# Optimization experiments

Hardware: AMD Instinct MI355X
Metric: run time of the kernel (lower is better)

## Reference

```python
import jax, jax.numpy as jnp
import numpy as np

EPS = 1e-8
LN_EPS = 1e-5
DIM, NHEADS = 512, 8
HEAD_DIM = DIM // NHEADS
SCALE = HEAD_DIM ** -0.5
ROLE_VOCAB = 8


def _layernorm(x, g, b):
    mu = x.mean(-1, keepdims=True)
    var = ((x - mu) ** 2).mean(-1, keepdims=True)
    return (x - mu) * jax.lax.rsqrt(var + LN_EPS) * g + b


def setup_inputs() -> dict:
    key = jax.random.key(0)
    ks = jax.random.split(key, 16)
    B, K, L, D = 8, 4, 1024, DIM
    s = 1.0 / np.sqrt(D)
    return {
        "state_repr": jax.random.normal(ks[0], (B, K, L, D), jnp.float32),
        "residue_mask": jax.random.randint(ks[1], (B, K, L), 0, 2) > 0,
        "state_weights": jax.random.uniform(ks[2], (B, K), jnp.float32),
        "state_roles": jax.random.randint(ks[3], (B, K), 0, ROLE_VOCAB),
        "state_present_mask": jnp.ones((B, K), dtype=bool),
        "role_emb": jax.random.normal(ks[4], (ROLE_VOCAB, D), jnp.float32),
        "Wq": jax.random.normal(ks[5], (D, D), jnp.float32) * s,
        "Wk": jax.random.normal(ks[6], (D, D), jnp.float32) * s,
        "Wv": jax.random.normal(ks[7], (D, D), jnp.float32) * s,
        "Wo": jax.random.normal(ks[8], (D, D), jnp.float32) * s,
        "ln1_g": jnp.ones((3 * D,), jnp.float32),
        "ln1_b": jnp.zeros((3 * D,), jnp.float32),
        "Wg1": jax.random.normal(ks[9], (D, 3 * D), jnp.float32) / np.sqrt(3 * D),
        "bg1": jnp.zeros((D,), jnp.float32),
        "Wg2": jax.random.normal(ks[10], (D, D), jnp.float32) * s,
        "bg2": jnp.zeros((D,), jnp.float32),
        "norm_g": jnp.ones((D,), jnp.float32),
        "norm_b": jnp.zeros((D,), jnp.float32),
    }


def _forward(state_repr, residue_mask, state_weights, state_roles, state_present_mask,
             role_emb, Wq, Wk, Wv, Wo, ln1_g, ln1_b, Wg1, bg1, Wg2, bg2, norm_g, norm_b):
    B, K, L, D = state_repr.shape
    H, hd = NHEADS, HEAD_DIM
    roles = jnp.maximum(state_roles, 0)
    role_e = role_emb[roles][:, :, None, :]                       # [B,K,1,D]
    valid = residue_mask & state_present_mask[:, :, None]          # [B,K,L]

    # normalized state weights
    pres = state_present_mask.astype(jnp.float32)
    w = state_weights.astype(jnp.float32) * pres
    denom = w.sum(1, keepdims=True)
    fallback = pres / jnp.maximum(pres.sum(1, keepdims=True), 1.0)
    nsw = jnp.where(denom > EPS, w / jnp.maximum(denom, EPS), fallback)  # [B,K]

    x = (state_repr + role_e) * valid[..., None]
    x = x.transpose(0, 2, 1, 3)                                    # [B,L,K,D]
    valid_rlk = valid.transpose(0, 2, 1)                           # [B,L,K]

    def proj(W):  # torch Linear: y = x @ W.T
        return (x @ W.T).reshape(B, L, K, H, hd).transpose(0, 1, 3, 2, 4)  # [B,L,H,K,hd]

    q, k, v = proj(Wq), proj(Wk), proj(Wv)
    logits = jnp.einsum('blhqd,blhkd->blhqk', q, k) * SCALE
    logits = logits + jnp.log(jnp.maximum(nsw, EPS))[:, None, None, None, :]
    key_mask = valid_rlk[:, :, None, None, :]                      # [B,L,1,1,K]
    logits = jnp.where(key_mask, logits, -jnp.inf)
    attn = jax.nn.softmax(logits, axis=-1)
    attn = jnp.nan_to_num(attn, nan=0.0, posinf=0.0, neginf=0.0)
    attn_out = jnp.einsum('blhqk,blhkd->blhqd', attn, v)
    attn_out = attn_out.transpose(0, 1, 3, 2, 4).reshape(B, L, K, D)
    attn_out = (attn_out @ Wo.T) * valid_rlk[..., None]

    swr = nsw[:, None, :] * valid_rlk.astype(jnp.float32)          # [B,L,K]
    swr = swr / jnp.maximum(swr.sum(-1, keepdims=True), EPS)
    weighted_mean = jnp.sum(x * swr[..., None], axis=2)            # [B,L,D]
    attn_pooled = jnp.sum(attn_out * swr[..., None], axis=2)

    max_in = jnp.where(valid_rlk[..., None], x, -1e9)
    max_feat = max_in.max(axis=2)
    has_any = valid_rlk.any(axis=2, keepdims=True)
    max_feat = jnp.where(has_any, max_feat, 0.0)

    fusion_base = 0.5 * (attn_pooled + weighted_mean)
    gate_in = jnp.concatenate([attn_pooled, weighted_mean, max_feat], axis=-1)
    h = _layernorm(gate_in, ln1_g, ln1_b)
    h = jax.nn.gelu(h @ Wg1.T + bg1, approximate=False)
    gate = jax.nn.sigmoid(h @ Wg2.T + bg2)
    fused = gate * fusion_base + (1.0 - gate) * max_feat
    fused = _layernorm(fused + weighted_mean, norm_g, norm_b)

    attn_mean = attn.mean(axis=(2, 3))                             # [B,L,K]
    return fused, attn_pooled, weighted_mean, max_feat, attn_mean, nsw


def reference(state_repr, residue_mask, state_weights, state_roles, state_present_mask,
              role_emb, Wq, Wk, Wv, Wo, ln1_g, ln1_b, Wg1, bg1, Wg2, bg2, norm_g, norm_b):
    return _forward(state_repr, residue_mask, state_weights, state_roles, state_present_mask,
                    role_emb, Wq, Wk, Wv, Wo, ln1_g, ln1_b, Wg1, bg1, Wg2, bg2, norm_g, norm_b)
```

## Files before the change

### kernel.cpp

```cpp
#include <hip/hip_runtime.h>
#include <math.h>

#define BB 8
#define KK 4
#define LL 1024
#define DD 512
#define HD 64
#define D3 1536
#define MM (BB*LL*KK)
#define BL (BB*LL)
#define SCALE 0.125f
#define EPSF 1e-8f
#define LN_EPSF 1e-5f

typedef _Float16 hfrag __attribute__((ext_vector_type(8)));
typedef float f32x4 __attribute__((ext_vector_type(4)));

__device__ __forceinline__ unsigned short f2h(float f) {
    _Float16 h = (_Float16)f;
    unsigned short u; __builtin_memcpy(&u, &h, 2); return u;
}
__device__ __forceinline__ float h2f(unsigned short u) {
    _Float16 h; __builtin_memcpy(&h, &u, 2); return (float)h;
}

__device__ __forceinline__ void glds16(const unsigned short* g, unsigned short* l) {
    __builtin_amdgcn_global_load_lds(
        (const __attribute__((address_space(1))) void*)g,
        (__attribute__((address_space(3))) void*)l, 16, 0, 0);
}

__device__ __forceinline__ void nsw_compute(const float* sw, const int* pres,
                                            int b, float* nswv) {
    float w[KK], pr[KK]; float denom = 0.f, ps = 0.f;
    #pragma unroll
    for (int k = 0; k < KK; ++k) {
        pr[k] = pres[b*KK + k] ? 1.f : 0.f;
        w[k]  = sw[b*KK + k] * pr[k];
        denom += w[k]; ps += pr[k];
    }
    #pragma unroll
    for (int k = 0; k < KK; ++k)
        nswv[k] = (denom > EPSF) ? w[k] / fmaxf(denom, EPSF)
                                 : pr[k] / fmaxf(ps, 1.f);
}

#define WSZ 262144
#define OG1 1048576
#define OG2 1835008
#define WTOT 2097152
__global__ __launch_bounds__(256) void cvt_weights(
        const float* __restrict__ Wq, const float* __restrict__ Wk,
        const float* __restrict__ Wv, const float* __restrict__ Wo,
        const float* __restrict__ Wg1, const float* __restrict__ Wg2,
        unsigned short* __restrict__ dst) {
    int t = blockIdx.x * 256 + threadIdx.x;
    int e = t * 4;
    const float* src; int off;
    if      (e < WSZ)    { src = Wq;  off = e; }
    else if (e < 2*WSZ)  { src = Wk;  off = e - WSZ; }
    else if (e < 3*WSZ)  { src = Wv;  off = e - 2*WSZ; }
    else if (e < OG1)    { src = Wo;  off = e - 3*WSZ; }
    else if (e < OG2)    { src = Wg1; off = e - OG1; }
    else                 { src = Wg2; off = e - OG2; }
    float4 v = *(const float4*)(src + off);
    ushort4 o;
    o.x = f2h(v.x); o.y = f2h(v.y); o.z = f2h(v.z); o.w = f2h(v.w);
    *(ushort4*)(dst + e) = o;
}

__global__ __launch_bounds__(256) void buildx_kernel(
        const float* __restrict__ SR, const int* __restrict__ residue,
        const int* __restrict__ pres, const int* __restrict__ roles,
        const float* __restrict__ role_emb, const float* __restrict__ sw,
        unsigned short* __restrict__ Xh, float* __restrict__ rowmask,
        float* __restrict__ out_wm, float* __restrict__ out_mx,
        float* __restrict__ f_nsw) {
    int t  = blockIdx.x * 256 + threadIdx.x;
    int bl = t >> 7;
    int d4 = (t & 127) << 2;
    int b  = bl >> 10, l = bl & 1023;
    float nswv[KK];
    nsw_compute(sw, pres, b, nswv);
    float mk[KK], swr[KK];
    float ssum = 0.f, many = 0.f;
    #pragma unroll
    for (int k = 0; k < KK; ++k) {
        int bk = b*KK + k;
        bool valid = (residue[(size_t)bk*LL + l] != 0) && (pres[bk] != 0);
        mk[k]  = valid ? 1.f : 0.f;
        swr[k] = nswv[k] * mk[k];
        ssum += swr[k]; many += mk[k];
    }
    float inv = 1.f / fmaxf(ssum, EPSF);
    bool hasany = many > 0.5f;
    float wmx = 0.f, wmy = 0.f, wmz = 0.f, wmw = 0.f;
    float mxx = -1e9f, mxy = -1e9f, mxz = -1e9f, mxw = -1e9f;
    #pragma unroll
    for (int k = 0; k < KK; ++k) {
        int bk = b*KK + k;
        int role = roles[bk]; if (role < 0) role = 0;
        float4 sr = *(const float4*)(SR + ((size_t)bk*LL + l)*DD + d4);
        float4 re = *(const float4*)(role_emb + (size_t)role*DD + d4);
        float xx = (sr.x + re.x)*mk[k], xy = (sr.y + re.y)*mk[k];
        float xz = (sr.z + re.z)*mk[k], xw = (sr.w + re.w)*mk[k];
        ushort4 xs; xs.x = f2h(xx); xs.y = f2h(xy); xs.z = f2h(xz); xs.w = f2h(xw);
        *(ushort4*)(Xh + (size_t)(bl*KK + k)*DD + d4) = xs;
        float s = swr[k]*inv;
        wmx = fmaf(xx, s, wmx); wmy = fmaf(xy, s, wmy);
        wmz = fmaf(xz, s, wmz); wmw = fmaf(xw, s, wmw);
        if (mk[k] > 0.5f) {
            mxx = fmaxf(mxx, xx); mxy = fmaxf(mxy, xy);
            mxz = fmaxf(mxz, xz); mxw = fmaxf(mxw, xw);
        }
    }
    if (!hasany) { mxx = mxy = mxz = mxw = 0.f; }
    float4 wmv; wmv.x = wmx; wmv.y = wmy; wmv.z = wmz; wmv.w = wmw;
    float4 mxv; mxv.x = mxx; mxv.y = mxy; mxv.z = mxz; mxv.w = mxw;
    *(float4*)(out_wm + (size_t)bl*DD + d4) = wmv;
    *(float4*)(out_mx + (size_t)bl*DD + d4) = mxv;
    if (d4 == 0) {
        #pragma unroll
        for (int k = 0; k < KK; ++k) rowmask[bl*KK + k] = mk[k];
    }
    if (blockIdx.x == 0 && threadIdx.x < BB*KK) {
        int bb = threadIdx.x >> 2, kk2 = threadIdx.x & 3;
        float nv[KK];
        nsw_compute(sw, pres, bb, nv);
        f_nsw[threadIdx.x] = nv[kk2];
    }
}

__global__ __launch_bounds__(512, 4) void gemm_qkv_8p(
        const unsigned short* __restrict__ A, const unsigned short* __restrict__ W,
        unsigned short* __restrict__ Cbase) {
    __shared__ __align__(16) unsigned short smem[36864];
    const int tid  = threadIdx.x;
    const int wave = tid >> 6, lane = tid & 63;
    const int id = blockIdx.x;
    const int wg = (id & 7) * 192 + (id >> 3);
    const int m0 = (wg / 12) * 256;
    const int n0 = (wg % 12) * 128;
    const int wm = wave >> 1, wn = wave & 1;
    const int fr = lane & 15, q = lane >> 4;
    const int srow = tid >> 2, scc = tid & 3;
    const int sswz = (scc ^ ((srow >> 1) & 3)) << 3;
    const unsigned short* Ag0 = A + (size_t)(m0 + srow)*512 + sswz;
    const unsigned short* Ag1 = Ag0 + (size_t)128*512;
    const unsigned short* Wg0 = W + (size_t)(n0 + srow)*512 + sswz;
    const int lA0 = tid << 3;
    const int lA1 = (tid + 512) << 3;
    int aoff[4], boff[4];
    #pragma unroll
    for (int mf = 0; mf < 4; ++mf) {
        int row = (wm << 6) + (mf << 4) + fr;
        aoff[mf] = (row << 5) + ((q ^ ((row >> 1) & 3)) << 3);
    }
    #pragma unroll
    for (int nf = 0; nf < 4; ++nf) {
        int row = (wn << 6) + (nf << 4) + fr;
        boff[nf] = (row << 5) + ((q ^ ((row >> 1) & 3)) << 3);
    }
    f32x4 acc[4][4] = {};

#define VMWAIT(N) asm volatile("s_waitcnt vmcnt(" #N ")" ::: "memory")
#define STAGE(tt) do { unsigned short* _d = smem + ((tt) % 3) * 12288; \
        const int _ko = (tt) << 5; \
        glds16(Ag0 + _ko, _d + lA0); glds16(Ag1 + _ko, _d + lA1); \
        glds16(Wg0 + _ko, _d + 8192 + lA0); } while (0)
#define MFROW(ai, areg) \
        acc[ai][0] = __builtin_amdgcn_mfma_f32_16x16x32_f16(areg, b0, acc[ai][0], 0, 0, 0); \
        acc[ai][1] = __builtin_amdgcn_mfma_f32_16x16x32_f16(areg, b1, acc[ai][1], 0, 0, 0); \
        acc[ai][2] = __builtin_amdgcn_mfma_f32_16x16x32_f16(areg, b2, acc[ai][2], 0, 0, 0); \
        acc[ai][3] = __builtin_amdgcn_mfma_f32_16x16x32_f16(areg, b3, acc[ai][3], 0, 0, 0);
#define TILE(t, STG, VM) do { \
        const unsigned short* _Ab = smem + ((t) % 3) * 12288; \
        const unsigned short* _Bb = _Ab + 8192; \
        VMWAIT(VM); \
        __builtin_amdgcn_s_barrier(); \
        __builtin_amdgcn_sched_barrier(0); \
        hfrag b0 = *(const hfrag*)(_Bb + boff[0]); \
        hfrag b1 = *(const hfrag*)(_Bb + boff[1]); \
        hfrag b2 = *(const hfrag*)(_Bb + boff[2]); \
        hfrag b3 = *(const hfrag*)(_Bb + boff[3]); \
        hfrag a0_ = *(const hfrag*)(_Ab + aoff[0]); \
        hfrag a1_ = *(const hfrag*)(_Ab + aoff[1]); \
        hfrag a2_ = *(const hfrag*)(_Ab + aoff[2]); \
        hfrag a3_ = *(const hfrag*)(_Ab + aoff[3]); \
        if (STG) STAGE((t) + 2); \
        __builtin_amdgcn_s_setprio(1); \
        MFROW(0, a0_) MFROW(1, a1_) MFROW(2, a2_) MFROW(3, a3_) \
        __builtin_amdgcn_s_setprio(0); \
    } while (0)

    STAGE(0); STAGE(1);
    #pragma unroll
    for (int t = 0; t < 14; ++t) TILE(t, 1, 3);
    TILE(14, 0, 3);
    TILE(15, 0, 0);
#undef TILE
#undef MFROW
#undef STAGE
#undef VMWAIT

    const int gc0 = n0 + (wn << 6);
    const int seg = gc0 >> 9;
    unsigned short* Cs = Cbase + (size_t)seg * ((size_t)MM * 512);
    const int cb = gc0 & 511;
    #pragma unroll
    for (int mf = 0; mf < 4; ++mf) {
        const int grow = m0 + (wm << 6) + (mf << 4) + (q << 2);
        #pragma unroll
        for (int nf = 0; nf < 4; ++nf) {
            const int col = cb + (nf << 4) + fr;
            #pragma unroll
            for (int r = 0; r < 4; ++r)
                Cs[(size_t)(grow + r) * 512 + col] = f2h(acc[mf][nf][r]);
        }
    }
}

__global__ __launch_bounds__(256) void attn_kernel(
        const unsigned short* __restrict__ Qb, const unsigned short* __restrict__ Kb,
        const unsigned short* __restrict__ Vb,
        unsigned short* __restrict__ pooled,
        const float* __restrict__ sw, const int* __restrict__ pres,
        const float* __restrict__ rowmask,
        float* __restrict__ attn_mean_out) {
    __shared__ float att[128];
    __shared__ float wv[32];
    __shared__ float lw[KK], mk[KK], sp[KK];
    int bl = blockIdx.x, b = bl >> 10, mb = bl * KK;
    int tid = threadIdx.x;
    if (tid < KK) {
        float nv[KK];
        nsw_compute(sw, pres, b, nv);
        lw[tid] = logf(fmaxf(nv[tid], EPSF));
        float mkk[KK]; float ssum = 0.f;
        #pragma unroll
        for (int k = 0; k < KK; ++k) { mkk[k] = rowmask[mb + k]; ssum += nv[k]*mkk[k]; }
        mk[tid] = mkk[tid];
        sp[tid] = nv[tid]*mkk[tid] / fmaxf(ssum, EPSF);
    }
    __syncthreads();
    if (tid < 128) {
        int h = tid >> 4, i = (tid >> 2) & 3, j = tid & 3;
        const unsigned short* qp = Qb + (size_t)(mb + i)*DD + h*HD;
        const unsigned short* kp = Kb + (size_t)(mb + j)*DD + h*HD;
        float s = 0.f;
        #pragma unroll
        for (int c = 0; c < 8; ++c) {
            hfrag qv = *(const hfrag*)(qp + c*8);
            hfrag kv = *(const hfrag*)(kp + c*8);
            #pragma unroll
            for (int e = 0; e < 8; ++e)
                s = fmaf((float)qv[e], (float)kv[e], s);
        }
        float lg = s * SCALE + lw[j];
        att[tid] = (mk[j] > 0.5f) ? lg : -INFINITY;
    }
    __syncthreads();
    if (tid < 32) {
        int base = tid * 4;
        float l0 = att[base], l1 = att[base+1], l2 = att[base+2], l3 = att[base+3];
        float m = fmaxf(fmaxf(l0, l1), fmaxf(l2, l3));
        if (m == -INFINITY) {
            att[base] = att[base+1] = att[base+2] = att[base+3] = 0.f;
        } else {
            float e0 = expf(l0 - m), e1 = expf(l1 - m), e2 = expf(l2 - m), e3 = expf(l3 - m);
            float inv = 1.f / (e0 + e1 + e2 + e3);
            att[base] = e0*inv; att[base+1] = e1*inv; att[base+2] = e2*inv; att[base+3] = e3*inv;
        }
    }
    __syncthreads();
    if (tid < KK) {
        float s = 0.f;
        for (int hi = 0; hi < 32; ++hi) s += att[hi*4 + tid];
        attn_mean_out[(size_t)bl*KK + tid] = s * (1.f/32.f);
    }
    if (tid < 32) {
        int h = tid >> 2, j = tid & 3;
        wv[tid] = sp[0]*att[h*16 + 0*4 + j] + sp[1]*att[h*16 + 1*4 + j]
                + sp[2]*att[h*16 + 2*4 + j] + sp[3]*att[h*16 + 3*4 + j];
    }
    __syncthreads();
    {
        int d2 = tid << 1, h = d2 >> 6;
        float s0 = 0.f, s1 = 0.f;
        #pragma unroll
        for (int j = 0; j < KK; ++j) {
            float aj = wv[h*4 + j];
            ushort2 vvv = *(const ushort2*)(Vb + (size_t)(mb + j)*DD + d2);
            s0 = fmaf(aj, h2f(vvv.x), s0);
            s1 = fmaf(aj, h2f(vvv.y), s1);
        }
        ushort2 o; o.x = f2h(s0); o.y = f2h(s1);
        *(ushort2*)(pooled + (size_t)bl*DD + d2) = o;
    }
}

__global__ __launch_bounds__(256, 3) void ap_gemm(
        const unsigned short* __restrict__ A,
        const unsigned short* __restrict__ W,
        float* __restrict__ out_ap) {
    __shared__ __align__(16) unsigned short smem[24576];
    const int tid  = threadIdx.x;
    const int wave = tid >> 6, lane = tid & 63;
    const int id = blockIdx.x;
    const int wg = (id & 7) * 32 + (id >> 3);
    const int m0 = (wg >> 2) * 128;
    const int n0 = (wg & 3) * 128;
    const int wm = wave >> 1, wn = wave & 1;
    const int fr = lane & 15, q = lane >> 4;
    const int srow = tid >> 2, scc = tid & 3;
    const int sswz = (scc ^ ((srow >> 1) & 3)) << 3;
    const unsigned short* Ag0 = A + (size_t)(m0 + srow)*512 + sswz;
    const unsigned short* Ag1 = Ag0 + (size_t)64*512;
    const unsigned short* Wg0 = W + (size_t)(n0 + srow)*512 + sswz;
    const unsigned short* Wg1p = Wg0 + (size_t)64*512;
    const int lA0 = tid << 3;
    const int lA1 = (tid + 256) << 3;
    int aoff[4], boff[4];
    #pragma unroll
    for (int mf = 0; mf < 4; ++mf) {
        int row = (wm << 6) + (mf << 4) + fr;
        aoff[mf] = (row << 5) + ((q ^ ((row >> 1) & 3)) << 3);
    }
    #pragma unroll
    for (int nf = 0; nf < 4; ++nf) {
        int row = (wn << 6) + (nf << 4) + fr;
        boff[nf] = (row << 5) + ((q ^ ((row >> 1) & 3)) << 3);
    }
    f32x4 acc[4][4] = {};

#define VMWAIT(N) asm volatile("s_waitcnt vmcnt(" #N ")" ::: "memory")
#define STAGE(tt) do { unsigned short* _d = smem + ((tt) % 3) * 8192; \
        const int _ko = (tt) << 5; \
        glds16(Ag0 + _ko, _d + lA0); glds16(Ag1 + _ko, _d + lA1); \
        glds16(Wg0 + _ko, _d + 4096 + lA0); glds16(Wg1p + _ko, _d + 4096 + lA1); } while (0)
#define MFROW(ai, areg) \
        acc[ai][0] = __builtin_amdgcn_mfma_f32_16x16x32_f16(areg, b0, acc[ai][0], 0, 0, 0); \
        acc[ai][1] = __builtin_amdgcn_mfma_f32_16x16x32_f16(areg, b1, acc[ai][1], 0, 0, 0); \
        acc[ai][2] = __builtin_amdgcn_mfma_f32_16x16x32_f16(areg, b2, acc[ai][2], 0, 0, 0); \
        acc[ai][3] = __builtin_amdgcn_mfma_f32_16x16x32_f16(areg, b3, acc[ai][3], 0, 0, 0);
#define TILE(t, STG, VM) do { \
        const unsigned short* _Ab = smem + ((t) % 3) * 8192; \
        const unsigned short* _Bb = _Ab + 4096; \
        VMWAIT(VM); \
        __builtin_amdgcn_s_barrier(); \
        __builtin_amdgcn_sched_barrier(0); \
        hfrag b0 = *(const hfrag*)(_Bb + boff[0]); \
        hfrag b1 = *(const hfrag*)(_Bb + boff[1]); \
        hfrag b2 = *(const hfrag*)(_Bb + boff[2]); \
        hfrag b3 = *(const hfrag*)(_Bb + boff[3]); \
        hfrag a0_ = *(const hfrag*)(_Ab + aoff[0]); \
        hfrag a1_ = *(const hfrag*)(_Ab + aoff[1]); \
        hfrag a2_ = *(const hfrag*)(_Ab + aoff[2]); \
        hfrag a3_ = *(const hfrag*)(_Ab + aoff[3]); \
        if (STG) STAGE((t) + 2); \
        __builtin_amdgcn_s_setprio(1); \
        MFROW(0, a0_) MFROW(1, a1_) MFROW(2, a2_) MFROW(3, a3_) \
        __builtin_amdgcn_s_setprio(0); \
    } while (0)

    STAGE(0); STAGE(1);
    #pragma unroll
    for (int t = 0; t < 14; ++t) TILE(t, 1, 4);
    TILE(14, 0, 4);
    TILE(15, 0, 0);
#undef TILE
#undef MFROW
#undef STAGE
#undef VMWAIT

    #pragma unroll
    for (int mf = 0; mf < 4; ++mf) {
        const int grow = m0 + (wm << 6) + (mf << 4) + (q << 2);
        #pragma unroll
        for (int nf = 0; nf < 4; ++nf) {
            const int col = n0 + (wn << 6) + (nf << 4) + fr;
            #pragma unroll
            for (int r = 0; r < 4; ++r)
                out_ap[(size_t)(grow + r)*512 + col] = acc[mf][nf][r];
        }
    }
}

__global__ __launch_bounds__(256) void ln1_kernel(
        const float* __restrict__ ap, const float* __restrict__ wm,
        const float* __restrict__ mx, const float* __restrict__ g,
        const float* __restrict__ bvec, unsigned short* __restrict__ hin) {
    const int bl = blockIdx.x * 4 + (threadIdx.x >> 6);
    const int lane = threadIdx.x & 63;
    const int c0 = lane * 8;
    float4 v[3][2];
    const float* srcs[3] = { ap + (size_t)bl*512 + c0,
                             wm + (size_t)bl*512 + c0,
                             mx + (size_t)bl*512 + c0 };
    float s = 0.f, s2 = 0.f;
    #pragma unroll
    for (int sg = 0; sg < 3; ++sg) {
        v[sg][0] = *(const float4*)(srcs[sg]);
        v[sg][1] = *(const float4*)(srcs[sg] + 4);
        #pragma unroll
        for (int e = 0; e < 8; ++e) {
            float x = ((const float*)v[sg])[e];
            s += x; s2 += x*x;
        }
    }
    #pragma unroll
    for (int o = 1; o < 64; o <<= 1) {
        s  += __shfl_xor(s,  o, 64);
        s2 += __shfl_xor(s2, o, 64);
    }
    const float mu = s * (1.f/(float)D3);
    const float var = s2 * (1.f/(float)D3) - mu*mu;
    const float rstd = rsqrtf(var + LN_EPSF);
    #pragma unroll
    for (int sg = 0; sg < 3; ++sg) {
        const int gofs = sg*512 + c0;
        #pragma unroll
        for (int h = 0; h < 2; ++h) {
            float4 g4 = *(const float4*)(g + gofs + h*4);
            float4 b4 = *(const float4*)(bvec + gofs + h*4);
            const float* sv = (const float*)&v[sg][h];
            ushort4 o4;
            o4.x = f2h((sv[0]-mu)*rstd*g4.x + b4.x);
            o4.y = f2h((sv[1]-mu)*rstd*g4.y + b4.y);
            o4.z = f2h((sv[2]-mu)*rstd*g4.z + b4.z);
            o4.w = f2h((sv[3]-mu)*rstd*g4.w + b4.w);
            *(ushort4*)(hin + (size_t)bl*D3 + gofs + h*4) = o4;
        }
    }
}

__global__ __launch_bounds__(256, 3) void gemm_g1(
        const unsigned short* __restrict__ A, const unsigned short* __restrict__ W,
        unsigned short* __restrict__ C, const float* __restrict__ bias) {
    __shared__ __align__(16) unsigned short smem[24576];
    const int tid  = threadIdx.x;
    const int wave = tid >> 6, lane = tid & 63;
    const int id = blockIdx.x;
    const int wg = (id & 7) * 32 + (id >> 3);
    const int m0 = (wg >> 2) * 128;
    const int n0 = (wg & 3) * 128;
    const int wm = wave >> 1, wn = wave & 1;
    const int fr = lane & 15, q = lane >> 4;
    const int srow = tid >> 2, scc = tid & 3;
    const int sswz = (scc ^ ((srow >> 1) & 3)) << 3;
    const unsigned short* Ag0 = A + (size_t)(m0 + srow)*D3 + sswz;
    const unsigned short* Ag1 = Ag0 + (size_t)64*D3;
    const unsigned short* Wg0 = W + (size_t)(n0 + srow)*D3 + sswz;
    const unsigned short* Wg1p = Wg0 + (size_t)64*D3;
    const int lA0 = tid << 3;
    const int lA1 = (tid + 256) << 3;
    int aoff[4], boff[4];
    #pragma unroll
    for (int mf = 0; mf < 4; ++mf) {
        int row = (wm << 6) + (mf << 4) + fr;
        aoff[mf] = (row << 5) + ((q ^ ((row >> 1) & 3)) << 3);
    }
    #pragma unroll
    for (int nf = 0; nf < 4; ++nf) {
        int row = (wn << 6) + (nf << 4) + fr;
        boff[nf] = (row << 5) + ((q ^ ((row >> 1) & 3)) << 3);
    }
    f32x4 acc[4][4] = {};

#define VMWAIT(N) asm volatile("s_waitcnt vmcnt(" #N ")" ::: "memory")
#define STAGE(tt) do { unsigned short* _d = smem + ((tt) % 3) * 8192; \
        const int _ko = (tt) << 5; \
        glds16(Ag0 + _ko, _d + lA0); glds16(Ag1 + _ko, _d + lA1); \
        glds16(Wg0 + _ko, _d + 4096 + lA0); glds16(Wg1p + _ko, _d + 4096 + lA1); } while (0)
#define MFROW(ai, areg) \
        acc[ai][0] = __builtin_amdgcn_mfma_f32_16x16x32_f16(areg, b0, acc[ai][0], 0, 0, 0); \
        acc[ai][1] = __builtin_amdgcn_mfma_f32_16x16x32_f16(areg, b1, acc[ai][1], 0, 0, 0); \
        acc[ai][2] = __builtin_amdgcn_mfma_f32_16x16x32_f16(areg, b2, acc[ai][2], 0, 0, 0); \
        acc[ai][3] = __builtin_amdgcn_mfma_f32_16x16x32_f16(areg, b3, acc[ai][3], 0, 0, 0);
#define TILE(t, STG, VM) do { \
        const unsigned short* _Ab = smem + ((t) % 3) * 8192; \
        const unsigned short* _Bb = _Ab + 4096; \
        VMWAIT(VM); \
        __builtin_amdgcn_s_barrier(); \
        __builtin_amdgcn_sched_barrier(0); \
        hfrag b0 = *(const hfrag*)(_Bb + boff[0]); \
        hfrag b1 = *(const hfrag*)(_Bb + boff[1]); \
        hfrag b2 = *(const hfrag*)(_Bb + boff[2]); \
        hfrag b3 = *(const hfrag*)(_Bb + boff[3]); \
        hfrag a0_ = *(const hfrag*)(_Ab + aoff[0]); \
        hfrag a1_ = *(const hfrag*)(_Ab + aoff[1]); \
        hfrag a2_ = *(const hfrag*)(_Ab + aoff[2]); \
        hfrag a3_ = *(const hfrag*)(_Ab + aoff[3]); \
        if (STG) STAGE((t) + 2); \
        __builtin_amdgcn_s_setprio(1); \
        MFROW(0, a0_) MFROW(1, a1_) MFROW(2, a2_) MFROW(3, a3_) \
        __builtin_amdgcn_s_setprio(0); \
    } while (0)

    STAGE(0); STAGE(1);
    #pragma unroll 3
    for (int t = 0; t < 46; ++t) TILE(t, 1, 4);
    TILE(46, 0, 4);
    TILE(47, 0, 0);
#undef TILE
#undef MFROW
#undef STAGE
#undef VMWAIT

    #pragma unroll
    for (int mf = 0; mf < 4; ++mf) {
        const int grow = m0 + (wm << 6) + (mf << 4) + (q << 2);
        #pragma unroll
        for (int nf = 0; nf < 4; ++nf) {
            const int col = n0 + (wn << 6) + (nf << 4) + fr;
            const float bv = bias[col];
            #pragma unroll
            for (int r = 0; r < 4; ++r) {
                float v = acc[mf][nf][r] + bv;
                v = 0.5f * v * (1.f + erff(v * 0.70710678118654752f));
                C[(size_t)(grow + r) * 512 + col] = f2h(v);
            }
        }
    }
}

__global__ __launch_bounds__(256, 3) void wg2_gemm(
        const unsigned short* __restrict__ A,
        const unsigned short* __restrict__ W,
        const float* __restrict__ bg2,
        const float* __restrict__ in_ap, const float* __restrict__ in_wm,
        const float* __restrict__ in_mx, float* __restrict__ pre) {
    __shared__ __align__(16) unsigned short smem[24576];
    const int tid  = threadIdx.x;
    const int wave = tid >> 6, lane = tid & 63;
    const int id = blockIdx.x;
    const int wg = (id & 7) * 32 + (id >> 3);
    const int m0 = (wg >> 2) * 128;
    const int n0 = (wg & 3) * 128;
    const int wm = wave >> 1, wn = wave & 1;
    const int fr = lane & 15, q = lane >> 4;
    const int srow = tid >> 2, scc = tid & 3;
    const int sswz = (scc ^ ((srow >> 1) & 3)) << 3;
    const unsigned short* Ag0 = A + (size_t)(m0 + srow)*512 + sswz;
    const unsigned short* Ag1 = Ag0 + (size_t)64*512;
    const unsigned short* Wg0 = W + (size_t)(n0 + srow)*512 + sswz;
    const unsigned short* Wg1p = Wg0 + (size_t)64*512;
    const int lA0 = tid << 3;
    const int lA1 = (tid + 256) << 3;
    int aoff[4], boff[4];
    #pragma unroll
    for (int mf = 0; mf < 4; ++mf) {
        int row = (wm << 6) + (mf << 4) + fr;
        aoff[mf] = (row << 5) + ((q ^ ((row >> 1) & 3)) << 3);
    }
    #pragma unroll
    for (int nf = 0; nf < 4; ++nf) {
        int row = (wn << 6) + (nf << 4) + fr;
        boff[nf] = (row << 5) + ((q ^ ((row >> 1) & 3)) << 3);
    }
    f32x4 acc[4][4] = {};

#define VMWAIT(N) asm volatile("s_waitcnt vmcnt(" #N ")" ::: "memory")
#define STAGE(tt) do { unsigned short* _d = smem + ((tt) % 3) * 8192; \
        const int _ko = (tt) << 5; \
        glds16(Ag0 + _ko, _d + lA0); glds16(Ag1 + _ko, _d + lA1); \
        glds16(Wg0 + _ko, _d + 4096 + lA0); glds16(Wg1p + _ko, _d + 4096 + lA1); } while (0)
#define MFROW(ai, areg) \
        acc[ai][0] = __builtin_amdgcn_mfma_f32_16x16x32_f16(areg, b0, acc[ai][0], 0, 0, 0); \
        acc[ai][1] = __builtin_amdgcn_mfma_f32_16x16x32_f16(areg, b1, acc[ai][1], 0, 0, 0); \
        acc[ai][2] = __builtin_amdgcn_mfma_f32_16x16x32_f16(areg, b2, acc[ai][2], 0, 0, 0); \
        acc[ai][3] = __builtin_amdgcn_mfma_f32_16x16x32_f16(areg, b3, acc[ai][3], 0, 0, 0);
#define TILE(t, STG, VM) do { \
        const unsigned short* _Ab = smem + ((t) % 3) * 8192; \
        const unsigned short* _Bb = _Ab + 4096; \
        VMWAIT(VM); \
        __builtin_amdgcn_s_barrier(); \
        __builtin_amdgcn_sched_barrier(0); \
        hfrag b0 = *(const hfrag*)(_Bb + boff[0]); \
        hfrag b1 = *(const hfrag*)(_Bb + boff[1]); \
        hfrag b2 = *(const hfrag*)(_Bb + boff[2]); \
        hfrag b3 = *(const hfrag*)(_Bb + boff[3]); \
        hfrag a0_ = *(const hfrag*)(_Ab + aoff[0]); \
        hfrag a1_ = *(const hfrag*)(_Ab + aoff[1]); \
        hfrag a2_ = *(const hfrag*)(_Ab + aoff[2]); \
        hfrag a3_ = *(const hfrag*)(_Ab + aoff[3]); \
        if (STG) STAGE((t) + 2); \
        __builtin_amdgcn_s_setprio(1); \
        MFROW(0, a0_) MFROW(1, a1_) MFROW(2, a2_) MFROW(3, a3_) \
        __builtin_amdgcn_s_setprio(0); \
    } while (0)

    STAGE(0); STAGE(1);
    #pragma unroll
    for (int t = 0; t < 14; ++t) TILE(t, 1, 4);
    TILE(14, 0, 4);
    TILE(15, 0, 0);
#undef TILE
#undef MFROW
#undef STAGE
#undef VMWAIT

    #pragma unroll
    for (int mf = 0; mf < 4; ++mf) {
        const int grow = m0 + (wm << 6) + (mf << 4) + (q << 2);
        #pragma unroll
        for (int nf = 0; nf < 4; ++nf) {
            const int col = n0 + (wn << 6) + (nf << 4) + fr;
            const float bv = bg2[col];
            #pragma unroll
            for (int r = 0; r < 4; ++r) {
                const int row = grow + r;
                float g = 1.f / (1.f + expf(-(acc[mf][nf][r] + bv)));
                float ap = in_ap[(size_t)row*512 + col];
                float wmv = in_wm[(size_t)row*512 + col];
                float mxv = in_mx[(size_t)row*512 + col];
                pre[(size_t)row*512 + col] = g*0.5f*(ap + wmv) + (1.f - g)*mxv + wmv;
            }
        }
    }
}

__global__ __launch_bounds__(256) void final_ln_kernel(
        const float* __restrict__ pre, const float* __restrict__ ng,
        const float* __restrict__ nb, float* __restrict__ fused) {
    const int row = blockIdx.x * 4 + (threadIdx.x >> 6);
    const int lane = threadIdx.x & 63;
    const int c0 = lane * 8;
    float4 p0 = *(const float4*)(pre + (size_t)row*512 + c0);
    float4 p1 = *(const float4*)(pre + (size_t)row*512 + c0 + 4);
    float s = 0.f, s2 = 0.f;
    const float* pv = (const float*)&p0;
    #pragma unroll
    for (int e = 0; e < 4; ++e) { s += pv[e]; s2 += pv[e]*pv[e]; }
    pv = (const float*)&p1;
    #pragma unroll
    for (int e = 0; e < 4; ++e) { s += pv[e]; s2 += pv[e]*pv[e]; }
    #pragma unroll
    for (int o = 1; o < 64; o <<= 1) {
        s  += __shfl_xor(s,  o, 64);
        s2 += __shfl_xor(s2, o, 64);
    }
    const float mu = s * (1.f/(float)DD);
    const float var = s2 * (1.f/(float)DD) - mu*mu;
    const float rstd = rsqrtf(var + LN_EPSF);
    float4 g0 = *(const float4*)(ng + c0), g1 = *(const float4*)(ng + c0 + 4);
    float4 b0 = *(const float4*)(nb + c0), b1 = *(const float4*)(nb + c0 + 4);
    float4 o0, o1;
    o0.x = (p0.x-mu)*rstd*g0.x + b0.x; o0.y = (p0.y-mu)*rstd*g0.y + b0.y;
    o0.z = (p0.z-mu)*rstd*g0.z + b0.z; o0.w = (p0.w-mu)*rstd*g0.w + b0.w;
    o1.x = (p1.x-mu)*rstd*g1.x + b1.x; o1.y = (p1.y-mu)*rstd*g1.y + b1.y;
    o1.z = (p1.z-mu)*rstd*g1.z + b1.z; o1.w = (p1.w-mu)*rstd*g1.w + b1.w;
    *(float4*)(fused + (size_t)row*512 + c0) = o0;
    *(float4*)(fused + (size_t)row*512 + c0 + 4) = o1;
}

extern "C" void kernel_launch(void* const* d_in, const int* in_sizes, int n_in,
                              void* d_out, int out_size, void* d_ws, size_t ws_size,
                              hipStream_t stream) {
    const float* SR      = (const float*)d_in[0];
    const int*   residue = (const int*)d_in[1];
    const float* sw      = (const float*)d_in[2];
    const int*   roles   = (const int*)d_in[3];
    const int*   pres    = (const int*)d_in[4];
    const float* role_emb= (const float*)d_in[5];
    const float* Wq      = (const float*)d_in[6];
    const float* Wk      = (const float*)d_in[7];
    const float* Wv      = (const float*)d_in[8];
    const float* Wo      = (const float*)d_in[9];
    const float* ln1_g   = (const float*)d_in[10];
    const float* ln1_b   = (const float*)d_in[11];
    const float* Wg1     = (const float*)d_in[12];
    const float* bg1     = (const float*)d_in[13];
    const float* Wg2     = (const float*)d_in[14];
    const float* bg2     = (const float*)d_in[15];
    const float* norm_g  = (const float*)d_in[16];
    const float* norm_b  = (const float*)d_in[17];

    float* out = (float*)d_out;
    const size_t BLD = (size_t)BL * DD;
    float* f_fused = out;
    float* f_ap    = out + BLD;
    float* f_wm    = out + 2*BLD;
    float* f_mx    = out + 3*BLD;
    float* f_am    = out + 4*BLD;
    float* f_nsw   = out + 4*BLD + (size_t)BL*KK;

    char* base = (char*)d_ws;
    const size_t MD2 = (size_t)MM * DD * 2;
    unsigned short* Xh = (unsigned short*)(base);
    unsigned short* Qh = (unsigned short*)(base + MD2);
    unsigned short* Kh = (unsigned short*)(base + 2*MD2);
    unsigned short* Vh = (unsigned short*)(base + 3*MD2);
    unsigned short* Wb = (unsigned short*)(base + 4*MD2);
    float* rmask = (float*)(base + 4*MD2 + (size_t)WTOT*2);
    unsigned short* PVh  = Xh;
    unsigned short* Hin  = Vh;
    unsigned short* Hbuf = Xh;
    float* preb = (float*)Kh;
    const unsigned short* Wqkv = Wb;
    const unsigned short* Woh  = Wb + 3*WSZ;
    const unsigned short* Wg1h = Wb + OG1;
    const unsigned short* Wg2h = Wb + OG2;

    dim3 blk(256);

    cvt_weights<<<WTOT/1024, blk, 0, stream>>>(Wq, Wk, Wv, Wo, Wg1, Wg2, Wb);
    buildx_kernel<<<(BL*128)/256, blk, 0, stream>>>(SR, residue, pres, roles, role_emb,
                                                    sw, Xh, rmask, f_wm, f_mx, f_nsw);

    gemm_qkv_8p<<<dim3(1536), dim3(512), 0, stream>>>(Xh, Wqkv, Qh);

    attn_kernel<<<BL, blk, 0, stream>>>(Qh, Kh, Vh, PVh, sw, pres, rmask, f_am);

    ap_gemm<<<dim3(256), blk, 0, stream>>>(PVh, Woh, f_ap);

    ln1_kernel<<<dim3(BL/4), blk, 0, stream>>>(
        f_ap, f_wm, f_mx, ln1_g, ln1_b, Hin);

    gemm_g1<<<dim3(256), blk, 0, stream>>>(Hin, Wg1h, Hbuf, bg1);

    wg2_gemm<<<dim3(256), blk, 0, stream>>>(
        Hbuf, Wg2h, bg2, f_ap, f_wm, f_mx, preb);

    final_ln_kernel<<<dim3(BL/4), blk, 0, stream>>>(
        preb, norm_g, norm_b, f_fused);
}
```

Baseline: 314.3 us.

## Use 64x64 tiles for the three tail GEMMs and batch two rows per attention block

Replaces the three 128x128-tile tail GEMMs (output projection, gate layer 1, gate layer 2) with one templated 64x64-tile kernel that launches 1024 blocks instead of 256. The aim is to fill all compute units of the MI355X, since 256 blocks leave many CUs idle. The attention kernel now handles two (b,l) rows per block so all 256 threads do work, and the V pooling uses wider loads. Smaller tiles give less data reuse per block and put more pressure on global and L2 bandwidth.

```diff
diff --git a/kernel.cpp b/kernel.cpp
--- a/kernel.cpp
+++ b/kernel.cpp
@@ -220,6 +220,101 @@
     }
 }
 
+template<int KT, int EPI>
+__global__ __launch_bounds__(256, 4) void gemm_tail(
+        const unsigned short* __restrict__ A, const unsigned short* __restrict__ W,
+        void* __restrict__ Cv, const float* __restrict__ bias,
+        const float* __restrict__ in_ap, const float* __restrict__ in_wm,
+        const float* __restrict__ in_mx) {
+    constexpr int K = KT * 32;
+    __shared__ __align__(16) unsigned short smem[12288];
+    const int tid  = threadIdx.x;
+    const int wave = tid >> 6, lane = tid & 63;
+    const int id = blockIdx.x;
+    const int wg = (id & 7) * 128 + (id >> 3);
+    const int m0 = (wg >> 3) * 64;
+    const int n0 = (wg & 7) * 64;
+    const int wm = wave >> 1, wn = wave & 1;
+    const int fr = lane & 15, q = lane >> 4;
+    const int srow = tid >> 2, scc = tid & 3;
+    const int sswz = (scc ^ ((srow >> 1) & 3)) << 3;
+    const unsigned short* Ag = A + (size_t)(m0 + srow)*K + sswz;
+    const unsigned short* Wg = W + (size_t)(n0 + srow)*K + sswz;
+    const int lA = tid << 3;
+    const int lB = 2048 + (tid << 3);
+    int aoff[2], boff[2];
+    #pragma unroll
+    for (int mf = 0; mf < 2; ++mf) {
+        int row = (wm << 5) + (mf << 4) + fr;
+        aoff[mf] = (row << 5) + ((q ^ ((row >> 1) & 3)) << 3);
+    }
+    #pragma unroll
+    for (int nf = 0; nf < 2; ++nf) {
+        int row = (wn << 5) + (nf << 4) + fr;
+        boff[nf] = 2048 + (row << 5) + ((q ^ ((row >> 1) & 3)) << 3);
+    }
+    f32x4 acc[2][2] = {};
+
+#define VMWAIT(N) asm volatile("s_waitcnt vmcnt(" #N ")" ::: "memory")
+#define STAGE(tt) do { unsigned short* _d = smem + ((tt) % 3) * 4096; \
+        const int _ko = (tt) << 5; \
+        glds16(Ag + _ko, _d + lA); glds16(Wg + _ko, _d + lB); } while (0)
+#define TILE(t, STG, VM) do { \
+        const unsigned short* _Ab = smem + ((t) % 3) * 4096; \
+        VMWAIT(VM); \
+        __builtin_amdgcn_s_barrier(); \
+        __builtin_amdgcn_sched_barrier(0); \
+        hfrag b0 = *(const hfrag*)(_Ab + boff[0]); \
+        hfrag b1 = *(const hfrag*)(_Ab + boff[1]); \
+        hfrag a0_ = *(const hfrag*)(_Ab + aoff[0]); \
+        hfrag a1_ = *(const hfrag*)(_Ab + aoff[1]); \
+        if (STG) STAGE((t) + 2); \
+        __builtin_amdgcn_s_setprio(1); \
+        acc[0][0] = __builtin_amdgcn_mfma_f32_16x16x32_f16(a0_, b0, acc[0][0], 0, 0, 0); \
+        acc[0][1] = __builtin_amdgcn_mfma_f32_16x16x32_f16(a0_, b1, acc[0][1], 0, 0, 0); \
+        acc[1][0] = __builtin_amdgcn_mfma_f32_16x16x32_f16(a1_, b0, acc[1][0], 0, 0, 0); \
+        acc[1][1] = __builtin_amdgcn_mfma_f32_16x16x32_f16(a1_, b1, acc[1][1], 0, 0, 0); \
+        __builtin_amdgcn_s_setprio(0); \
+    } while (0)
+
+    STAGE(0); STAGE(1);
+    #pragma unroll 3
+    for (int t = 0; t < KT - 2; ++t) TILE(t, 1, 2);
+    TILE(KT - 2, 0, 2);
+    TILE(KT - 1, 0, 0);
+#undef TILE
+#undef STAGE
+#undef VMWAIT
+
+    #pragma unroll
+    for (int mf = 0; mf < 2; ++mf) {
+        const int grow = m0 + (wm << 5) + (mf << 4) + (q << 2);
+        #pragma unroll
+        for (int nf = 0; nf < 2; ++nf) {
+            const int col = n0 + (wn << 5) + (nf << 4) + fr;
+            #pragma unroll
+            for (int r = 0; r < 4; ++r) {
+                const int row = grow + r;
+                float v = acc[mf][nf][r];
+                if (EPI == 0) {
+                    ((float*)Cv)[(size_t)row*512 + col] = v;
+                } else if (EPI == 1) {
+                    v += bias[col];
+                    v = 0.5f * v * (1.f + erff(v * 0.70710678118654752f));
+                    ((unsigned short*)Cv)[(size_t)row*512 + col] = f2h(v);
+                } else {
+                    float g = 1.f / (1.f + expf(-(v + bias[col])));
+                    float ap = in_ap[(size_t)row*512 + col];
+                    float wmv = in_wm[(size_t)row*512 + col];
+                    float mxv = in_mx[(size_t)row*512 + col];
+                    ((float*)Cv)[(size_t)row*512 + col] =
+                        g*0.5f*(ap + wmv) + (1.f - g)*mxv + wmv;
+                }
+            }
+        }
+    }
+}
+
 __global__ __launch_bounds__(256) void attn_kernel(
         const unsigned short* __restrict__ Qb, const unsigned short* __restrict__ Kb,
         const unsigned short* __restrict__ Vb,
@@ -227,24 +322,31 @@
         const float* __restrict__ sw, const int* __restrict__ pres,
         const float* __restrict__ rowmask,
         float* __restrict__ attn_mean_out) {
-    __shared__ float att[128];
-    __shared__ float wv[32];
-    __shared__ float lw[KK], mk[KK], sp[KK];
-    int bl = blockIdx.x, b = bl >> 10, mb = bl * KK;
-    int tid = threadIdx.x;
-    if (tid < KK) {
+    __shared__ float att[2][128];
+    __shared__ float wv[2][32];
+    __shared__ float lw[2][KK], mk[2][KK], sp[2][KK];
+    const int blp = blockIdx.x * 2;
+    const int tid = threadIdx.x;
+    if (tid < 8) {
+        const int blq = tid >> 2, k = tid & 3;
+        const int bl = blp + blq, b = bl >> 10;
         float nv[KK];
         nsw_compute(sw, pres, b, nv);
-        lw[tid] = logf(fmaxf(nv[tid], EPSF));
+        lw[blq][k] = logf(fmaxf(nv[k], EPSF));
         float mkk[KK]; float ssum = 0.f;
         #pragma unroll
-        for (int k = 0; k < KK; ++k) { mkk[k] = rowmask[mb + k]; ssum += nv[k]*mkk[k]; }
-        mk[tid] = mkk[tid];
-        sp[tid] = nv[tid]*mkk[tid] / fmaxf(ssum, EPSF);
+        for (int kk = 0; kk < KK; ++kk) {
+            mkk[kk] = rowmask[bl*KK + kk];
+            ssum += nv[kk]*mkk[kk];
+        }
+        mk[blq][k] = mkk[k];
+        sp[blq][k] = nv[k]*mkk[k] / fmaxf(ssum, EPSF);
     }
     __syncthreads();
-    if (tid < 128) {
-        int h = tid >> 4, i = (tid >> 2) & 3, j = tid & 3;
+    {
+        const int blq = tid >> 7, t2 = tid & 127;
+        const int h = t2 >> 4, i = (t2 >> 2) & 3, j = t2 & 3;
+        const int mb = (blp + blq) * KK;
         const unsigned short* qp = Qb + (size_t)(mb + i)*DD + h*HD;
         const unsigned short* kp = Kb + (size_t)(mb + j)*DD + h*HD;
         float s = 0.f;
@@ -256,133 +358,55 @@
             for (int e = 0; e < 8; ++e)
                 s = fmaf((float)qv[e], (float)kv[e], s);
         }
-        float lg = s * SCALE + lw[j];
-        att[tid] = (mk[j] > 0.5f) ? lg : -INFINITY;
+        float lg = s * SCALE + lw[blq][j];
+        att[blq][t2] = (mk[blq][j] > 0.5f) ? lg : -INFINITY;
     }
     __syncthreads();
-    if (tid < 32) {
-        int base = tid * 4;
-        float l0 = att[base], l1 = att[base+1], l2 = att[base+2], l3 = att[base+3];
+    if (tid < 64) {
+        const int blq = tid >> 5, t2 = tid & 31;
+        float* ab = &att[blq][t2 * 4];
+        float l0 = ab[0], l1 = ab[1], l2 = ab[2], l3 = ab[3];
         float m = fmaxf(fmaxf(l0, l1), fmaxf(l2, l3));
         if (m == -INFINITY) {
-            att[base] = att[base+1] = att[base+2] = att[base+3] = 0.f;
+            ab[0] = ab[1] = ab[2] = ab[3] = 0.f;
         } else {
             float e0 = expf(l0 - m), e1 = expf(l1 - m), e2 = expf(l2 - m), e3 = expf(l3 - m);
             float inv = 1.f / (e0 + e1 + e2 + e3);
-            att[base] = e0*inv; att[base+1] = e1*inv; att[base+2] = e2*inv; att[base+3] = e3*inv;
+            ab[0] = e0*inv; ab[1] = e1*inv; ab[2] = e2*inv; ab[3] = e3*inv;
         }
     }
     __syncthreads();
-    if (tid < KK) {
+    if (tid < 8) {
+        const int blq = tid >> 2, k = tid & 3;
         float s = 0.f;
-        for (int hi = 0; hi < 32; ++hi) s += att[hi*4 + tid];
-        attn_mean_out[(size_t)bl*KK + tid] = s * (1.f/32.f);
-    }
-    if (tid < 32) {
-        int h = tid >> 2, j = tid & 3;
-        wv[tid] = sp[0]*att[h*16 + 0*4 + j] + sp[1]*att[h*16 + 1*4 + j]
-                + sp[2]*att[h*16 + 2*4 + j] + sp[3]*att[h*16 + 3*4 + j];
+        for (int hi = 0; hi < 32; ++hi) s += att[blq][hi*4 + k];
+        attn_mean_out[(size_t)(blp + blq)*KK + k] = s * (1.f/32.f);
+    }
+    if (tid < 64) {
+        const int blq = tid >> 5, t2 = tid & 31;
+        const int h = t2 >> 2, j = t2 & 3;
+        wv[blq][t2] = sp[blq][0]*att[blq][h*16 + 0*4 + j]
+                    + sp[blq][1]*att[blq][h*16 + 1*4 + j]
+                    + sp[blq][2]*att[blq][h*16 + 2*4 + j]
+                    + sp[blq][3]*att[blq][h*16 + 3*4 + j];
     }
     __syncthreads();
     {
-        int d2 = tid << 1, h = d2 >> 6;
-        float s0 = 0.f, s1 = 0.f;
+        const int blq = tid >> 7, t2 = tid & 127;
+        const int d4 = t2 << 2, h = d4 >> 6;
+        const int mb = (blp + blq) * KK;
+        float s0 = 0.f, s1 = 0.f, s2 = 0.f, s3 = 0.f;
         #pragma unroll
         for (int j = 0; j < KK; ++j) {
-            float aj = wv[h*4 + j];
-            ushort2 vvv = *(const ushort2*)(Vb + (size_t)(mb + j)*DD + d2);
-            s0 = fmaf(aj, h2f(vvv.x), s0);
-            s1 = fmaf(aj, h2f(vvv.y), s1);
-        }
-        ushort2 o; o.x = f2h(s0); o.y = f2h(s1);
-        *(ushort2*)(pooled + (size_t)bl*DD + d2) = o;
-    }
-}
-
-__global__ __launch_bounds__(256, 3) void ap_gemm(
-        const unsigned short* __restrict__ A,
-        const unsigned short* __restrict__ W,
-        float* __restrict__ out_ap) {
-    __shared__ __align__(16) unsigned short smem[24576];
-    const int tid  = threadIdx.x;
-    const int wave = tid >> 6, lane = tid & 63;
-    const int id = blockIdx.x;
-    const int wg = (id & 7) * 32 + (id >> 3);
-    const int m0 = (wg >> 2) * 128;
-    const int n0 = (wg & 3) * 128;
-    const int wm = wave >> 1, wn = wave & 1;
-    const int fr = lane & 15, q = lane >> 4;
-    const int srow = tid >> 2, scc = tid & 3;
-    const int sswz = (scc ^ ((srow >> 1) & 3)) << 3;
-    const unsigned short* Ag0 = A + (size_t)(m0 + srow)*512 + sswz;
-    const unsigned short* Ag1 = Ag0 + (size_t)64*512;
-    const unsigned short* Wg0 = W + (size_t)(n0 + srow)*512 + sswz;
-    const unsigned short* Wg1p = Wg0 + (size_t)64*512;
-    const int lA0 = tid << 3;
-    const int lA1 = (tid + 256) << 3;
-    int aoff[4], boff[4];
-    #pragma unroll
-    for (int mf = 0; mf < 4; ++mf) {
-        int row = (wm << 6) + (mf << 4) + fr;
-        aoff[mf] = (row << 5) + ((q ^ ((row >> 1) & 3)) << 3);
-    }
-    #pragma unroll
-    for (int nf = 0; nf < 4; ++nf) {
-        int row = (wn << 6) + (nf << 4) + fr;
-        boff[nf] = (row << 5) + ((q ^ ((row >> 1) & 3)) << 3);
-    }
-    f32x4 acc[4][4] = {};
-
-#define VMWAIT(N) asm volatile("s_waitcnt vmcnt(" #N ")" ::: "memory")
-#define STAGE(tt) do { unsigned short* _d = smem + ((tt) % 3) * 8192; \
-        const int _ko = (tt) << 5; \
-        glds16(Ag0 + _ko, _d + lA0); glds16(Ag1 + _ko, _d + lA1); \
-        glds16(Wg0 + _ko, _d + 4096 + lA0); glds16(Wg1p + _ko, _d + 4096 + lA1); } while (0)
-#define MFROW(ai, areg) \
-        acc[ai][0] = __builtin_amdgcn_mfma_f32_16x16x32_f16(areg, b0, acc[ai][0], 0, 0, 0); \
-        acc[ai][1] = __builtin_amdgcn_mfma_f32_16x16x32_f16(areg, b1, acc[ai][1], 0, 0, 0); \
-        acc[ai][2] = __builtin_amdgcn_mfma_f32_16x16x32_f16(areg, b2, acc[ai][2], 0, 0, 0); \
-        acc[ai][3] = __builtin_amdgcn_mfma_f32_16x16x32_f16(areg, b3, acc[ai][3], 0, 0, 0);
-#define TILE(t, STG, VM) do { \
-        const unsigned short* _Ab = smem + ((t) % 3) * 8192; \
-        const unsigned short* _Bb = _Ab + 4096; \
-        VMWAIT(VM); \
-        __builtin_amdgcn_s_barrier(); \
-        __builtin_amdgcn_sched_barrier(0); \
-        hfrag b0 = *(const hfrag*)(_Bb + boff[0]); \
-        hfrag b1 = *(const hfrag*)(_Bb + boff[1]); \
-        hfrag b2 = *(const hfrag*)(_Bb + boff[2]); \
-        hfrag b3 = *(const hfrag*)(_Bb + boff[3]); \
-        hfrag a0_ = *(const hfrag*)(_Ab + aoff[0]); \
-        hfrag a1_ = *(const hfrag*)(_Ab + aoff[1]); \
-        hfrag a2_ = *(const hfrag*)(_Ab + aoff[2]); \
-        hfrag a3_ = *(const hfrag*)(_Ab + aoff[3]); \
-        if (STG) STAGE((t) + 2); \
-        __builtin_amdgcn_s_setprio(1); \
-        MFROW(0, a0_) MFROW(1, a1_) MFROW(2, a2_) MFROW(3, a3_) \
-        __builtin_amdgcn_s_setprio(0); \
-    } while (0)
-
-    STAGE(0); STAGE(1);
-    #pragma unroll
-    for (int t = 0; t < 14; ++t) TILE(t, 1, 4);
-    TILE(14, 0, 4);
-    TILE(15, 0, 0);
-#undef TILE
-#undef MFROW
-#undef STAGE
-#undef VMWAIT
-
-    #pragma unroll
-    for (int mf = 0; mf < 4; ++mf) {
-        const int grow = m0 + (wm << 6) + (mf << 4) + (q << 2);
-        #pragma unroll
-        for (int nf = 0; nf < 4; ++nf) {
-            const int col = n0 + (wn << 6) + (nf << 4) + fr;
-            #pragma unroll
-            for (int r = 0; r < 4; ++r)
-                out_ap[(size_t)(grow + r)*512 + col] = acc[mf][nf][r];
-        }
+            float aj = wv[blq][h*4 + j];
+            ushort4 vv = *(const ushort4*)(Vb + (size_t)(mb + j)*DD + d4);
+            s0 = fmaf(aj, h2f(vv.x), s0);
+            s1 = fmaf(aj, h2f(vv.y), s1);
+            s2 = fmaf(aj, h2f(vv.z), s2);
+            s3 = fmaf(aj, h2f(vv.w), s3);
+        }
+        ushort4 o; o.x = f2h(s0); o.y = f2h(s1); o.z = f2h(s2); o.w = f2h(s3);
+        *(ushort4*)(pooled + (size_t)(blp + blq)*DD + d4) = o;
     }
 }
 
@@ -430,192 +454,6 @@
             o4.z = f2h((sv[2]-mu)*rstd*g4.z + b4.z);
             o4.w = f2h((sv[3]-mu)*rstd*g4.w + b4.w);
             *(ushort4*)(hin + (size_t)bl*D3 + gofs + h*4) = o4;
-        }
-    }
-}
-
-__global__ __launch_bounds__(256, 3) void gemm_g1(
-        const unsigned short* __restrict__ A, const unsigned short* __restrict__ W,
-        unsigned short* __restrict__ C, const float* __restrict__ bias) {
-    __shared__ __align__(16) unsigned short smem[24576];
-    const int tid  = threadIdx.x;
-    const int wave = tid >> 6, lane = tid & 63;
-    const int id = blockIdx.x;
-    const int wg = (id & 7) * 32 + (id >> 3);
-    const int m0 = (wg >> 2) * 128;
-    const int n0 = (wg & 3) * 128;
-    const int wm = wave >> 1, wn = wave & 1;
-    const int fr = lane & 15, q = lane >> 4;
-    const int srow = tid >> 2, scc = tid & 3;
-    const int sswz = (scc ^ ((srow >> 1) & 3)) << 3;
-    const unsigned short* Ag0 = A + (size_t)(m0 + srow)*D3 + sswz;
-    const unsigned short* Ag1 = Ag0 + (size_t)64*D3;
-    const unsigned short* Wg0 = W + (size_t)(n0 + srow)*D3 + sswz;
-    const unsigned short* Wg1p = Wg0 + (size_t)64*D3;
-    const int lA0 = tid << 3;
-    const int lA1 = (tid + 256) << 3;
-    int aoff[4], boff[4];
-    #pragma unroll
-    for (int mf = 0; mf < 4; ++mf) {
-        int row = (wm << 6) + (mf << 4) + fr;
-        aoff[mf] = (row << 5) + ((q ^ ((row >> 1) & 3)) << 3);
-    }
-    #pragma unroll
-    for (int nf = 0; nf < 4; ++nf) {
-        int row = (wn << 6) + (nf << 4) + fr;
-        boff[nf] = (row << 5) + ((q ^ ((row >> 1) & 3)) << 3);
-    }
-    f32x4 acc[4][4] = {};
-
-#define VMWAIT(N) asm volatile("s_waitcnt vmcnt(" #N ")" ::: "memory")
-#define STAGE(tt) do { unsigned short* _d = smem + ((tt) % 3) * 8192; \
-        const int _ko = (tt) << 5; \
-        glds16(Ag0 + _ko, _d + lA0); glds16(Ag1 + _ko, _d + lA1); \
-        glds16(Wg0 + _ko, _d + 4096 + lA0); glds16(Wg1p + _ko, _d + 4096 + lA1); } while (0)
-#define MFROW(ai, areg) \
-        acc[ai][0] = __builtin_amdgcn_mfma_f32_16x16x32_f16(areg, b0, acc[ai][0], 0, 0, 0); \
-        acc[ai][1] = __builtin_amdgcn_mfma_f32_16x16x32_f16(areg, b1, acc[ai][1], 0, 0, 0); \
-        acc[ai][2] = __builtin_amdgcn_mfma_f32_16x16x32_f16(areg, b2, acc[ai][2], 0, 0, 0); \
-        acc[ai][3] = __builtin_amdgcn_mfma_f32_16x16x32_f16(areg, b3, acc[ai][3], 0, 0, 0);
-#define TILE(t, STG, VM) do { \
-        const unsigned short* _Ab = smem + ((t) % 3) * 8192; \
-        const unsigned short* _Bb = _Ab + 4096; \
-        VMWAIT(VM); \
-        __builtin_amdgcn_s_barrier(); \
-        __builtin_amdgcn_sched_barrier(0); \
-        hfrag b0 = *(const hfrag*)(_Bb + boff[0]); \
-        hfrag b1 = *(const hfrag*)(_Bb + boff[1]); \
-        hfrag b2 = *(const hfrag*)(_Bb + boff[2]); \
-        hfrag b3 = *(const hfrag*)(_Bb + boff[3]); \
-        hfrag a0_ = *(const hfrag*)(_Ab + aoff[0]); \
-        hfrag a1_ = *(const hfrag*)(_Ab + aoff[1]); \
-        hfrag a2_ = *(const hfrag*)(_Ab + aoff[2]); \
-        hfrag a3_ = *(const hfrag*)(_Ab + aoff[3]); \
-        if (STG) STAGE((t) + 2); \
-        __builtin_amdgcn_s_setprio(1); \
-        MFROW(0, a0_) MFROW(1, a1_) MFROW(2, a2_) MFROW(3, a3_) \
-        __builtin_amdgcn_s_setprio(0); \
-    } while (0)
-
-    STAGE(0); STAGE(1);
-    #pragma unroll 3
-    for (int t = 0; t < 46; ++t) TILE(t, 1, 4);
-    TILE(46, 0, 4);
-    TILE(47, 0, 0);
-#undef TILE
-#undef MFROW
-#undef STAGE
-#undef VMWAIT
-
-    #pragma unroll
-    for (int mf = 0; mf < 4; ++mf) {
-        const int grow = m0 + (wm << 6) + (mf << 4) + (q << 2);
-        #pragma unroll
-        for (int nf = 0; nf < 4; ++nf) {
-            const int col = n0 + (wn << 6) + (nf << 4) + fr;
-            const float bv = bias[col];
-            #pragma unroll
-            for (int r = 0; r < 4; ++r) {
-                float v = acc[mf][nf][r] + bv;
-                v = 0.5f * v * (1.f + erff(v * 0.70710678118654752f));
-                C[(size_t)(grow + r) * 512 + col] = f2h(v);
-            }
-        }
-    }
-}
-
-__global__ __launch_bounds__(256, 3) void wg2_gemm(
-        const unsigned short* __restrict__ A,
-        const unsigned short* __restrict__ W,
-        const float* __restrict__ bg2,
-        const float* __restrict__ in_ap, const float* __restrict__ in_wm,
-        const float* __restrict__ in_mx, float* __restrict__ pre) {
-    __shared__ __align__(16) unsigned short smem[24576];
-    const int tid  = threadIdx.x;
-    const int wave = tid >> 6, lane = tid & 63;
-    const int id = blockIdx.x;
-    const int wg = (id & 7) * 32 + (id >> 3);
-    const int m0 = (wg >> 2) * 128;
-    const int n0 = (wg & 3) * 128;
-    const int wm = wave >> 1, wn = wave & 1;
-    const int fr = lane & 15, q = lane >> 4;
-    const int srow = tid >> 2, scc = tid & 3;
-    const int sswz = (scc ^ ((srow >> 1) & 3)) << 3;
-    const unsigned short* Ag0 = A + (size_t)(m0 + srow)*512 + sswz;
-    const unsigned short* Ag1 = Ag0 + (size_t)64*512;
-    const unsigned short* Wg0 = W + (size_t)(n0 + srow)*512 + sswz;
-    const unsigned short* Wg1p = Wg0 + (size_t)64*512;
-    const int lA0 = tid << 3;
-    const int lA1 = (tid + 256) << 3;
-    int aoff[4], boff[4];
-    #pragma unroll
-    for (int mf = 0; mf < 4; ++mf) {
-        int row = (wm << 6) + (mf << 4) + fr;
-        aoff[mf] = (row << 5) + ((q ^ ((row >> 1) & 3)) << 3);
-    }
-    #pragma unroll
-    for (int nf = 0; nf < 4; ++nf) {
-        int row = (wn << 6) + (nf << 4) + fr;
-        boff[nf] = (row << 5) + ((q ^ ((row >> 1) & 3)) << 3);
-    }
-    f32x4 acc[4][4] = {};
-
-#define VMWAIT(N) asm volatile("s_waitcnt vmcnt(" #N ")" ::: "memory")
-#define STAGE(tt) do { unsigned short* _d = smem + ((tt) % 3) * 8192; \
-        const int _ko = (tt) << 5; \
-        glds16(Ag0 + _ko, _d + lA0); glds16(Ag1 + _ko, _d + lA1); \
-        glds16(Wg0 + _ko, _d + 4096 + lA0); glds16(Wg1p + _ko, _d + 4096 + lA1); } while (0)
-#define MFROW(ai, areg) \
-        acc[ai][0] = __builtin_amdgcn_mfma_f32_16x16x32_f16(areg, b0, acc[ai][0], 0, 0, 0); \
-        acc[ai][1] = __builtin_amdgcn_mfma_f32_16x16x32_f16(areg, b1, acc[ai][1], 0, 0, 0); \
-        acc[ai][2] = __builtin_amdgcn_mfma_f32_16x16x32_f16(areg, b2, acc[ai][2], 0, 0, 0); \
-        acc[ai][3] = __builtin_amdgcn_mfma_f32_16x16x32_f16(areg, b3, acc[ai][3], 0, 0, 0);
-#define TILE(t, STG, VM) do { \
-        const unsigned short* _Ab = smem + ((t) % 3) * 8192; \
-        const unsigned short* _Bb = _Ab + 4096; \
-        VMWAIT(VM); \
-        __builtin_amdgcn_s_barrier(); \
-        __builtin_amdgcn_sched_barrier(0); \
-        hfrag b0 = *(const hfrag*)(_Bb + boff[0]); \
-        hfrag b1 = *(const hfrag*)(_Bb + boff[1]); \
-        hfrag b2 = *(const hfrag*)(_Bb + boff[2]); \
-        hfrag b3 = *(const hfrag*)(_Bb + boff[3]); \
-        hfrag a0_ = *(const hfrag*)(_Ab + aoff[0]); \
-        hfrag a1_ = *(const hfrag*)(_Ab + aoff[1]); \
-        hfrag a2_ = *(const hfrag*)(_Ab + aoff[2]); \
-        hfrag a3_ = *(const hfrag*)(_Ab + aoff[3]); \
-        if (STG) STAGE((t) + 2); \
-        __builtin_amdgcn_s_setprio(1); \
-        MFROW(0, a0_) MFROW(1, a1_) MFROW(2, a2_) MFROW(3, a3_) \
-        __builtin_amdgcn_s_setprio(0); \
-    } while (0)
-
-    STAGE(0); STAGE(1);
-    #pragma unroll
-    for (int t = 0; t < 14; ++t) TILE(t, 1, 4);
-    TILE(14, 0, 4);
-    TILE(15, 0, 0);
-#undef TILE
-#undef MFROW
-#undef STAGE
-#undef VMWAIT
-
-    #pragma unroll
-    for (int mf = 0; mf < 4; ++mf) {
-        const int grow = m0 + (wm << 6) + (mf << 4) + (q << 2);
-        #pragma unroll
-        for (int nf = 0; nf < 4; ++nf) {
-            const int col = n0 + (wn << 6) + (nf << 4) + fr;
-            const float bv = bg2[col];
-            #pragma unroll
-            for (int r = 0; r < 4; ++r) {
-                const int row = grow + r;
-                float g = 1.f / (1.f + expf(-(acc[mf][nf][r] + bv)));
-                float ap = in_ap[(size_t)row*512 + col];
-                float wmv = in_wm[(size_t)row*512 + col];
-                float mxv = in_mx[(size_t)row*512 + col];
-                pre[(size_t)row*512 + col] = g*0.5f*(ap + wmv) + (1.f - g)*mxv + wmv;
-            }
         }
     }
 }
@@ -710,17 +548,19 @@
 
     gemm_qkv_8p<<<dim3(1536), dim3(512), 0, stream>>>(Xh, Wqkv, Qh);
 
-    attn_kernel<<<BL, blk, 0, stream>>>(Qh, Kh, Vh, PVh, sw, pres, rmask, f_am);
-
-    ap_gemm<<<dim3(256), blk, 0, stream>>>(PVh, Woh, f_ap);
+    attn_kernel<<<dim3(BL/2), blk, 0, stream>>>(Qh, Kh, Vh, PVh, sw, pres, rmask, f_am);
+
+    gemm_tail<16, 0><<<dim3(1024), blk, 0, stream>>>(
+        PVh, Woh, f_ap, nullptr, nullptr, nullptr, nullptr);
 
     ln1_kernel<<<dim3(BL/4), blk, 0, stream>>>(
         f_ap, f_wm, f_mx, ln1_g, ln1_b, Hin);
 
-    gemm_g1<<<dim3(256), blk, 0, stream>>>(Hin, Wg1h, Hbuf, bg1);
-
-    wg2_gemm<<<dim3(256), blk, 0, stream>>>(
-        Hbuf, Wg2h, bg2, f_ap, f_wm, f_mx, preb);
+    gemm_tail<48, 1><<<dim3(1024), blk, 0, stream>>>(
+        Hin, Wg1h, Hbuf, bg1, nullptr, nullptr, nullptr);
+
+    gemm_tail<16, 2><<<dim3(1024), blk, 0, stream>>>(
+        Hbuf, Wg2h, preb, bg2, f_ap, f_wm, f_mx);
 
     final_ln_kernel<<<dim3(BL/4), blk, 0, stream>>>(
         preb, norm_g, norm_b, f_fused);
```

New measurement: 319.6 us. Within noise of the previous version (+1.7%).
